# Kernel tuning notes

Measured on AMD Instinct MI355X. Metric: run time of the kernel, lower is better.

## Reference

```python
import jax, jax.numpy as jnp
import numpy as np

DIM = 1024
DEPTH = 6
HEADS = 16
DIM_HEAD = 64
INNER = HEADS * DIM_HEAD  # 1024
NUM_LATENTS = 64
FF = 4 * DIM
EPS = 1e-5


def _ln(t, g, b):
    m = jnp.mean(t, axis=-1, keepdims=True)
    v = jnp.mean(jnp.square(t - m), axis=-1, keepdims=True)
    return (t - m) * jax.lax.rsqrt(v + EPS) * g + b


def setup_inputs() -> dict:
    key = jax.random.key(0)
    ks = jax.random.split(key, 12)
    s = 0.02
    x = jax.random.normal(ks[0], (4, 8, 4, 256, DIM), dtype=jnp.float32)
    latents = jax.random.normal(ks[1], (NUM_LATENTS, DIM), dtype=jnp.float32)
    wq = jax.random.normal(ks[2], (DEPTH, DIM, INNER), dtype=jnp.float32) * s
    wkv = jax.random.normal(ks[3], (DEPTH, DIM, 2 * INNER), dtype=jnp.float32) * s
    wo = jax.random.normal(ks[4], (DEPTH, INNER, DIM), dtype=jnp.float32) * s
    w1 = jax.random.normal(ks[5], (DEPTH, DIM, FF), dtype=jnp.float32) * s
    w2 = jax.random.normal(ks[6], (DEPTH, FF, DIM), dtype=jnp.float32) * s
    nm_g = jnp.ones((DEPTH, DIM), jnp.float32); nm_b = jnp.zeros((DEPTH, DIM), jnp.float32)
    nl_g = jnp.ones((DEPTH, DIM), jnp.float32); nl_b = jnp.zeros((DEPTH, DIM), jnp.float32)
    ff_g = jnp.ones((DEPTH, DIM), jnp.float32); ff_b = jnp.zeros((DEPTH, DIM), jnp.float32)
    fin_g = jnp.ones((DIM,), jnp.float32); fin_b = jnp.zeros((DIM,), jnp.float32)
    return {"x": x, "latents": latents, "nm_g": nm_g, "nm_b": nm_b,
            "nl_g": nl_g, "nl_b": nl_b, "wq": wq, "wkv": wkv, "wo": wo,
            "ff_g": ff_g, "ff_b": ff_b, "w1": w1, "w2": w2,
            "fin_g": fin_g, "fin_b": fin_b}


def _to_heads(t):
    # [B,T,N,inner] -> [B,h,T,N,dh]
    B, T, N, _ = t.shape
    return t.reshape(B, T, N, HEADS, DIM_HEAD).transpose(0, 3, 1, 2, 4)


def reference(x, latents, nm_g, nm_b, nl_g, nl_b, wq, wkv, wo,
              ff_g, ff_b, w1, w2, fin_g, fin_b):
    B, T, F, V, D = x.shape
    x = x.reshape(B, T, F * V, D)  # media tokens
    lat = jnp.broadcast_to(latents[None, None], (B, T, NUM_LATENTS, D))
    scale = DIM_HEAD ** -0.5
    for i in range(DEPTH):
        # --- cross attention (queries=latents, kv = media ++ latents) ---
        xn = _ln(x, nm_g[i], nm_b[i])
        ln_lat = _ln(lat, nl_g[i], nl_b[i])
        q = ln_lat @ wq[i]                                # [B,T,N2,inner]
        kv = jnp.concatenate([xn, ln_lat], axis=-2) @ wkv[i]
        k, v = jnp.split(kv, 2, axis=-1)
        qh = _to_heads(q) * scale                          # [B,h,T,N2,dh]
        kh = _to_heads(k)                                  # [B,h,T,Nk,dh]
        vh = _to_heads(v)
        sim = jnp.einsum('bhtid,bhtjd->bhtij', qh, kh)
        attn = jax.nn.softmax(sim, axis=-1)
        out = jnp.einsum('bhtij,bhtjd->bhtid', attn, vh)   # [B,h,T,N2,dh]
        out = out.transpose(0, 2, 3, 1, 4).reshape(B, T, NUM_LATENTS, INNER)
        lat = out @ wo[i] + lat
        # --- feed forward ---
        h = _ln(lat, ff_g[i], ff_b[i]) @ w1[i]
        h = jax.nn.gelu(h, approximate=False) @ w2[i]
        lat = h + lat
    return _ln(lat, fin_g, fin_b)
```

## Files before the change

### kernel.cpp

```cpp
#include <hip/hip_runtime.h>


typedef unsigned short u16;
typedef __attribute__((ext_vector_type(8))) short short8;
typedef __attribute__((ext_vector_type(4))) float f32x4;

__device__ __forceinline__ float bf2f(u16 u) {
  return __uint_as_float(((unsigned)u) << 16);
}
__device__ __forceinline__ u16 f2bf(float f) {
  unsigned u = __float_as_uint(f);
  unsigned r = (u + 0x7FFFu + ((u >> 16) & 1u)) >> 16;
  return (u16)r;
}

__global__ void detect_kernel(const u16* __restrict__ x, int* __restrict__ flag) {
  int lane = threadIdx.x;
  u16 u = x[2 * lane];
  int e = (u >> 7) & 0xFF;
  unsigned long long b = __ballot(e >= 115 && e <= 133);
  if (lane == 0) flag[0] = (__popcll(b) >= 40) ? 1 : 0;
}

__global__ __launch_bounds__(256)
void wtrans_kernel(const void* __restrict__ W, long woff, u16* __restrict__ Wt,
                   int K, int N, const int* __restrict__ flag) {
  const int isb = *flag;
  __shared__ u16 t[64][72];
  const long k0 = (long)blockIdx.x * 64;
  const long n0 = (long)blockIdx.y * 64;
  const int tr = threadIdx.x >> 2;
  const int tc = (threadIdx.x & 3) * 16;
  if (isb) {
    const u16* src = (const u16*)W + woff + (k0 + tr) * N + n0 + tc;
    *(int4*)&t[tr][tc]     = *(const int4*)src;
    *(int4*)&t[tr][tc + 8] = *(const int4*)(src + 8);
  } else {
    const float* src = (const float*)W + woff + (k0 + tr) * N + n0 + tc;
    float4 f0 = *(const float4*)(src);
    float4 f1 = *(const float4*)(src + 4);
    float4 f2 = *(const float4*)(src + 8);
    float4 f3 = *(const float4*)(src + 12);
    u16 tmp[16] = {f2bf(f0.x), f2bf(f0.y), f2bf(f0.z), f2bf(f0.w),
                   f2bf(f1.x), f2bf(f1.y), f2bf(f1.z), f2bf(f1.w),
                   f2bf(f2.x), f2bf(f2.y), f2bf(f2.z), f2bf(f2.w),
                   f2bf(f3.x), f2bf(f3.y), f2bf(f3.z), f2bf(f3.w)};
    *(int4*)&t[tr][tc]     = *(int4*)&tmp[0];
    *(int4*)&t[tr][tc + 8] = *(int4*)&tmp[8];
  }
  __syncthreads();
  u16 o[16];
#pragma unroll
  for (int j = 0; j < 16; ++j) o[j] = t[tc + j][tr];
  u16* dst = Wt + (n0 + tr) * (long)K + k0 + tc;
  *(int4*)dst       = *(int4*)&o[0];
  *(int4*)(dst + 8) = *(int4*)&o[8];
}

template <int EPI>
__global__ __launch_bounds__(256, 2)
void gemm_kernel(const u16* __restrict__ A, const u16* __restrict__ Bt,
                 void* __restrict__ Cp, const float* __restrict__ R,
                 int M, int N, int K) {
  __shared__ u16 As[128][74];
  __shared__ u16 Bs[128][74];

  const int tid  = threadIdx.x;
  const int lane = tid & 63;
  const int wave = tid >> 6;
  const int wm = (wave >> 1) * 64;
  const int wn = (wave & 1) * 64;
  const int r  = lane & 15;
  const int qd = lane >> 4;

  const long bm = (long)blockIdx.x * 128;
  const long bn = (long)blockIdx.y * 128;

  f32x4 acc[4][4];
#pragma unroll
  for (int i = 0; i < 4; ++i)
#pragma unroll
    for (int j = 0; j < 4; ++j) acc[i][j] = (f32x4){0.f, 0.f, 0.f, 0.f};

  const int ra = tid >> 3, ca = (tid & 7) * 8;
  const u16* Aptr = A  + (bm + ra) * (long)K + ca;
  const u16* Bptr = Bt + (bn + ra) * (long)K + ca;

  for (int k0 = 0; k0 < K; k0 += 64) {
#pragma unroll
    for (int it = 0; it < 4; ++it) {
      int4 av = *(const int4*)(Aptr + (long)(it * 32) * K + k0);
      *(int4*)(&As[ra + it * 32][ca]) = av;
    }
#pragma unroll
    for (int it = 0; it < 4; ++it) {
      int4 bv = *(const int4*)(Bptr + (long)(it * 32) * K + k0);
      *(int4*)(&Bs[ra + it * 32][ca]) = bv;
    }
    __syncthreads();

#pragma unroll
    for (int kh = 0; kh < 2; ++kh) {
      short8 af[4], bfv[4];
#pragma unroll
      for (int mt = 0; mt < 4; ++mt)
        af[mt] = *(const short8*)(&As[wm + mt * 16 + r][kh * 32 + qd * 8]);
#pragma unroll
      for (int nt = 0; nt < 4; ++nt)
        bfv[nt] = *(const short8*)(&Bs[wn + nt * 16 + r][kh * 32 + qd * 8]);
#pragma unroll
      for (int mt = 0; mt < 4; ++mt)
#pragma unroll
        for (int nt = 0; nt < 4; ++nt)
          acc[mt][nt] = __builtin_amdgcn_mfma_f32_16x16x32_bf16(
              bfv[nt], af[mt], acc[mt][nt], 0, 0, 0);
    }
    __syncthreads();
  }

#pragma unroll
  for (int mt = 0; mt < 4; ++mt) {
    const long row = bm + wm + mt * 16 + r;
#pragma unroll
    for (int nt = 0; nt < 4; ++nt) {
      const long col = bn + wn + nt * 16 + qd * 4;
      const long idx = row * N + col;
      if (EPI == 0) {
        ushort4 o;
        o.x = f2bf(acc[mt][nt][0]); o.y = f2bf(acc[mt][nt][1]);
        o.z = f2bf(acc[mt][nt][2]); o.w = f2bf(acc[mt][nt][3]);
        *(ushort4*)((u16*)Cp + idx) = o;
      } else if (EPI == 1) {
        ushort4 o;
        float v0 = acc[mt][nt][0], v1 = acc[mt][nt][1];
        float v2 = acc[mt][nt][2], v3 = acc[mt][nt][3];
        o.x = f2bf(0.5f * v0 * (1.0f + erff(v0 * 0.70710678118654752f)));
        o.y = f2bf(0.5f * v1 * (1.0f + erff(v1 * 0.70710678118654752f)));
        o.z = f2bf(0.5f * v2 * (1.0f + erff(v2 * 0.70710678118654752f)));
        o.w = f2bf(0.5f * v3 * (1.0f + erff(v3 * 0.70710678118654752f)));
        *(ushort4*)((u16*)Cp + idx) = o;
      } else {
        float4 rv = *(const float4*)(R + idx);
        float4 o;
        o.x = acc[mt][nt][0] + rv.x; o.y = acc[mt][nt][1] + rv.y;
        o.z = acc[mt][nt][2] + rv.z; o.w = acc[mt][nt][3] + rv.w;
        *(float4*)((float*)Cp + idx) = o;
      }
    }
  }
}

template <int INMODE, int OUTMODE>
__global__ __launch_bounds__(256)
void ln_kernel(const void* __restrict__ inp, long ioff,
               const void* __restrict__ gam, const void* __restrict__ bet,
               long goff, void* __restrict__ outp, const int* __restrict__ flag) {
  const int isb = *flag;
  const long row = blockIdx.x;
  const int tid = threadIdx.x;
  float x0, x1, x2, x3;
  const bool in_f32 = (INMODE == 1) || (!isb);
  if (in_f32) {
    float4 v = *((const float4*)((const float*)inp + ioff + row * 1024) + tid);
    x0 = v.x; x1 = v.y; x2 = v.z; x3 = v.w;
  } else {
    ushort4 u = *((const ushort4*)((const u16*)inp + ioff + row * 1024) + tid);
    x0 = bf2f(u.x); x1 = bf2f(u.y); x2 = bf2f(u.z); x3 = bf2f(u.w);
  }
  float s1 = x0 + x1 + x2 + x3;
  float s2 = x0 * x0 + x1 * x1 + x2 * x2 + x3 * x3;
#pragma unroll
  for (int off = 32; off >= 1; off >>= 1) {
    s1 += __shfl_xor(s1, off);
    s2 += __shfl_xor(s2, off);
  }
  __shared__ float r1[4], r2[4];
  if ((tid & 63) == 0) { r1[tid >> 6] = s1; r2[tid >> 6] = s2; }
  __syncthreads();
  s1 = r1[0] + r1[1] + r1[2] + r1[3];
  s2 = r2[0] + r2[1] + r2[2] + r2[3];
  const float mean = s1 * (1.0f / 1024.0f);
  const float var  = s2 * (1.0f / 1024.0f) - mean * mean;
  const float rstd = rsqrtf(var + 1e-5f);
  float g0, g1, g2, g3, b0, b1, b2, b3;
  if (isb) {
    ushort4 ug = *((const ushort4*)((const u16*)gam + goff) + tid);
    ushort4 ub = *((const ushort4*)((const u16*)bet + goff) + tid);
    g0 = bf2f(ug.x); g1 = bf2f(ug.y); g2 = bf2f(ug.z); g3 = bf2f(ug.w);
    b0 = bf2f(ub.x); b1 = bf2f(ub.y); b2 = bf2f(ub.z); b3 = bf2f(ub.w);
  } else {
    float4 vg = *((const float4*)((const float*)gam + goff) + tid);
    float4 vb = *((const float4*)((const float*)bet + goff) + tid);
    g0 = vg.x; g1 = vg.y; g2 = vg.z; g3 = vg.w;
    b0 = vb.x; b1 = vb.y; b2 = vb.z; b3 = vb.w;
  }
  float o0 = (x0 - mean) * rstd * g0 + b0;
  float o1 = (x1 - mean) * rstd * g1 + b1;
  float o2 = (x2 - mean) * rstd * g2 + b2;
  float o3 = (x3 - mean) * rstd * g3 + b3;
  const bool out_f32 = (OUTMODE == 1) && (!isb);
  if (out_f32) {
    float4 o = {o0, o1, o2, o3};
    *((float4*)((float*)outp + row * 1024) + tid) = o;
  } else {
    ushort4 o;
    o.x = f2bf(o0); o.y = f2bf(o1); o.z = f2bf(o2); o.w = f2bf(o3);
    *((ushort4*)((u16*)outp + row * 1024) + tid) = o;
  }
}

__global__ __launch_bounds__(256)
void init_lat_kernel(const void* __restrict__ latents, float* __restrict__ lat,
                     const int* __restrict__ flag) {
  const int isb = *flag;
  long i = (long)blockIdx.x * 256 + threadIdx.x;
  long src = (4 * i) & 65535;
  float4 o;
  if (isb) {
    ushort4 u = *(const ushort4*)((const u16*)latents + src);
    o = (float4){bf2f(u.x), bf2f(u.y), bf2f(u.z), bf2f(u.w)};
  } else {
    o = *(const float4*)((const float*)latents + src);
  }
  *(float4*)(lat + 4 * i) = o;
}

__global__ __launch_bounds__(256, 2)
void attn_kernel(const u16* __restrict__ Q, const u16* __restrict__ KVM,
                 const u16* __restrict__ KVL, u16* __restrict__ O, int g0) {
  const int gl = blockIdx.x;
  const int g  = g0 + gl;
  const int h  = blockIdx.y;
  __shared__ u16 k_s[64][72];
  __shared__ u16 vt_s[64][72];
  __shared__ u16 qp_s[64][72];

  const int tid  = threadIdx.x;
  const int lane = tid & 63;
  const int wave = tid >> 6;
  const int r  = lane & 15;
  const int qd = lane >> 4;
  const int qr = wave * 16;

  {
    const int rr = tid >> 2, cc = (tid & 3) * 16;
    const u16* qp = Q + ((long)g * 64 + rr) * 1024 + h * 64 + cc;
    *(int4*)&qp_s[rr][cc]     = *(const int4*)qp;
    *(int4*)&qp_s[rr][cc + 8] = *(const int4*)(qp + 8);
  }
  __syncthreads();

  short8 aq0 = *(const short8*)&qp_s[qr + r][qd * 8];
  short8 aq1 = *(const short8*)&qp_s[qr + r][32 + qd * 8];

  f32x4 acc_o[4];
  float m0[4], l0[4];
#pragma unroll
  for (int i = 0; i < 4; ++i) {
    m0[i] = -3.0e38f;
    l0[i] = 0.f;
    acc_o[i] = (f32x4){0.f, 0.f, 0.f, 0.f};
  }

  for (int t = 0; t < 17; ++t) {
    const u16* base = (t < 16)
        ? KVM + ((long)gl * 1024 + t * 64) * 2048 + h * 64
        : KVL + ((long)g * 64) * 2048 + h * 64;
    {
      const int rr = tid >> 2, cc = (tid & 3) * 16;
      const u16* kp = base + (long)rr * 2048 + cc;
      *(int4*)&k_s[rr][cc]     = *(const int4*)kp;
      *(int4*)&k_s[rr][cc + 8] = *(const int4*)(kp + 8);
    }
    {
      const int d = lane;
      const u16* vp = base + 1024 + (long)(wave * 16) * 2048 + d;
      union { u16 u[16]; int4 v[2]; } tmp;
#pragma unroll
      for (int u = 0; u < 16; ++u) tmp.u[u] = vp[(long)u * 2048];
      *(int4*)&vt_s[d][wave * 16]     = tmp.v[0];
      *(int4*)&vt_s[d][wave * 16 + 8] = tmp.v[1];
    }
    __syncthreads();

    f32x4 sac[4];
#pragma unroll
    for (int nt = 0; nt < 4; ++nt) sac[nt] = (f32x4){0.f, 0.f, 0.f, 0.f};
#pragma unroll
    for (int nt = 0; nt < 4; ++nt) {
      short8 b0 = *(const short8*)&k_s[nt * 16 + r][qd * 8];
      short8 b1 = *(const short8*)&k_s[nt * 16 + r][32 + qd * 8];
      sac[nt] = __builtin_amdgcn_mfma_f32_16x16x32_bf16(aq0, b0, sac[nt], 0, 0, 0);
      sac[nt] = __builtin_amdgcn_mfma_f32_16x16x32_bf16(aq1, b1, sac[nt], 0, 0, 0);
    }

    float pr[4][4];
#pragma unroll
    for (int nt = 0; nt < 4; ++nt)
#pragma unroll
      for (int i = 0; i < 4; ++i) pr[nt][i] = sac[nt][i] * 0.125f;

#pragma unroll
    for (int i = 0; i < 4; ++i) {
      float mt = fmaxf(fmaxf(pr[0][i], pr[1][i]), fmaxf(pr[2][i], pr[3][i]));
      mt = fmaxf(mt, __shfl_xor(mt, 1));
      mt = fmaxf(mt, __shfl_xor(mt, 2));
      mt = fmaxf(mt, __shfl_xor(mt, 4));
      mt = fmaxf(mt, __shfl_xor(mt, 8));
      float mn = fmaxf(m0[i], mt);
      float al = __expf(m0[i] - mn);
      m0[i] = mn;
      float ts = 0.f;
#pragma unroll
      for (int nt = 0; nt < 4; ++nt) {
        float p = __expf(pr[nt][i] - mn);
        pr[nt][i] = p;
        ts += p;
      }
      ts += __shfl_xor(ts, 1);
      ts += __shfl_xor(ts, 2);
      ts += __shfl_xor(ts, 4);
      ts += __shfl_xor(ts, 8);
      l0[i] = l0[i] * al + ts;
#pragma unroll
      for (int nt = 0; nt < 4; ++nt) acc_o[nt][i] *= al;
    }

#pragma unroll
    for (int nt = 0; nt < 4; ++nt)
#pragma unroll
      for (int i = 0; i < 4; ++i)
        qp_s[qr + qd * 4 + i][nt * 16 + r] = f2bf(pr[nt][i]);

    short8 ap0 = *(const short8*)&qp_s[qr + r][qd * 8];
    short8 ap1 = *(const short8*)&qp_s[qr + r][32 + qd * 8];
#pragma unroll
    for (int nt = 0; nt < 4; ++nt) {
      short8 b0 = *(const short8*)&vt_s[nt * 16 + r][qd * 8];
      short8 b1 = *(const short8*)&vt_s[nt * 16 + r][32 + qd * 8];
      acc_o[nt] = __builtin_amdgcn_mfma_f32_16x16x32_bf16(ap0, b0, acc_o[nt], 0, 0, 0);
      acc_o[nt] = __builtin_amdgcn_mfma_f32_16x16x32_bf16(ap1, b1, acc_o[nt], 0, 0, 0);
    }
    __syncthreads();
  }

#pragma unroll
  for (int i = 0; i < 4; ++i) {
    float inv = 1.0f / l0[i];
    long row = (long)g * 64 + qr + qd * 4 + i;
#pragma unroll
    for (int nt = 0; nt < 4; ++nt)
      O[row * 1024 + h * 64 + nt * 16 + r] = f2bf(acc_o[nt][i] * inv);
  }
}

extern "C" void kernel_launch(void* const* d_in, const int* in_sizes, int n_in,
                              void* d_out, int out_size, void* d_ws, size_t ws_size,
                              hipStream_t stream) {
  const void* x     = d_in[0];
  const void* lats  = d_in[1];
  const void* nm_g  = d_in[2];
  const void* nm_b  = d_in[3];
  const void* nl_g  = d_in[4];
  const void* nl_b  = d_in[5];
  const void* wq    = d_in[6];
  const void* wkv   = d_in[7];
  const void* wo    = d_in[8];
  const void* ff_g  = d_in[9];
  const void* ff_b  = d_in[10];
  const void* w1    = d_in[11];
  const void* w2    = d_in[12];
  const void* fin_g = d_in[13];
  const void* fin_b = d_in[14];

  const size_t MB = 1024ull * 1024ull;
  char* w = (char*)d_ws;
  int*   flag = (int*)w;    w += 1 * MB;
  float* lat  = (float*)w;  w += 8 * MB;
  u16*   lnl  = (u16*)w;    w += 4 * MB;
  u16*   qbuf = (u16*)w;    w += 4 * MB;
  u16*   ao   = (u16*)w;    w += 4 * MB;
  u16*   kvl  = (u16*)w;    w += 8 * MB;
  u16*   h1   = (u16*)w;    w += 16 * MB;
  u16*   wqt  = (u16*)w;    w += 2 * MB;
  u16*   wkvt = (u16*)w;    w += 4 * MB;
  u16*   wot  = (u16*)w;    w += 2 * MB;
  u16*   w1t  = (u16*)w;    w += 8 * MB;
  u16*   w2t  = (u16*)w;    w += 8 * MB;
  const size_t base = 69 * MB;
  int CH = 32;
  while (CH > 1 && base + (size_t)CH * 6 * MB > ws_size) CH >>= 1;
  u16* xn  = (u16*)w;  w += (size_t)CH * 2 * MB;
  u16* kvm = (u16*)w;
  const int nch = 32 / CH;

  detect_kernel<<<1, 64, 0, stream>>>((const u16*)x, flag);
  init_lat_kernel<<<2048, 256, 0, stream>>>(lats, lat, flag);

  for (int i = 0; i < 6; ++i) {
    wtrans_kernel<<<dim3(16, 16), 256, 0, stream>>>(
        wq, (long)i * 1024 * 1024, wqt, 1024, 1024, flag);
    wtrans_kernel<<<dim3(16, 32), 256, 0, stream>>>(
        wkv, (long)i * 1024 * 2048, wkvt, 1024, 2048, flag);
    wtrans_kernel<<<dim3(16, 16), 256, 0, stream>>>(
        wo, (long)i * 1024 * 1024, wot, 1024, 1024, flag);
    wtrans_kernel<<<dim3(16, 64), 256, 0, stream>>>(
        w1, (long)i * 1024 * 4096, w1t, 1024, 4096, flag);
    wtrans_kernel<<<dim3(64, 16), 256, 0, stream>>>(
        w2, (long)i * 4096 * 1024, w2t, 4096, 1024, flag);

    ln_kernel<1, 0><<<2048, 256, 0, stream>>>(
        lat, 0, nl_g, nl_b, (long)i * 1024, lnl, flag);
    gemm_kernel<0><<<dim3(16, 8), 256, 0, stream>>>(
        lnl, wqt, qbuf, nullptr, 2048, 1024, 1024);
    gemm_kernel<0><<<dim3(16, 16), 256, 0, stream>>>(
        lnl, wkvt, kvl, nullptr, 2048, 2048, 1024);
    for (int c = 0; c < nch; ++c) {
      ln_kernel<0, 0><<<CH * 1024, 256, 0, stream>>>(
          x, (long)c * CH * 1024 * 1024, nm_g, nm_b, (long)i * 1024, xn, flag);
      gemm_kernel<0><<<dim3(CH * 8, 16), 256, 0, stream>>>(
          xn, wkvt, kvm, nullptr, CH * 1024, 2048, 1024);
      attn_kernel<<<dim3(CH, 16), 256, 0, stream>>>(qbuf, kvm, kvl, ao, c * CH);
    }
    gemm_kernel<2><<<dim3(16, 8), 256, 0, stream>>>(
        ao, wot, lat, lat, 2048, 1024, 1024);
    ln_kernel<1, 0><<<2048, 256, 0, stream>>>(
        lat, 0, ff_g, ff_b, (long)i * 1024, lnl, flag);
    gemm_kernel<1><<<dim3(16, 32), 256, 0, stream>>>(
        lnl, w1t, h1, nullptr, 2048, 4096, 1024);
    gemm_kernel<2><<<dim3(16, 8), 256, 0, stream>>>(
        h1, w2t, lat, lat, 2048, 1024, 4096);
  }
  ln_kernel<1, 1><<<2048, 256, 0, stream>>>(
      lat, 0, fin_g, fin_b, 0, d_out, flag);
}
```

Measured before the change: 3.503 ms.

## Prefetch next K-tile into registers and swizzle GEMM block order

The GEMM main loop now loads the next 64-wide K slice of A and B into registers while MFMAs run on the current shared-memory tile, then writes it to shared memory after a barrier. This hides global-memory latency behind compute. Block indices are also remapped into groups of 8 along M so blocks running at the same time share B tiles in L2. The register prefetch adds 32 VGPRs per thread, which may pressure the launch bound of 2 blocks per SM.

After: 9.573 ms. 2.73x slower.

```diff
diff --git a/kernel.cpp b/kernel.cpp
--- a/kernel.cpp
+++ b/kernel.cpp
@@ -73,8 +73,17 @@
   const int r  = lane & 15;
   const int qd = lane >> 4;
 
-  const long bm = (long)blockIdx.x * 128;
-  const long bn = (long)blockIdx.y * 128;
+  int bx = blockIdx.x, by = blockIdx.y;
+  if ((gridDim.x & 7) == 0) {
+    const int gy = gridDim.y;
+    int f = by * gridDim.x + bx;
+    int ntg = 8 * gy;
+    int g = f / ntg, rem = f % ntg;
+    bx = g * 8 + (rem & 7);
+    by = rem >> 3;
+  }
+  const long bm = (long)bx * 128;
+  const long bn = (long)by * 128;
 
   f32x4 acc[4][4];
 #pragma unroll
@@ -86,18 +95,28 @@
   const u16* Aptr = A  + (bm + ra) * (long)K + ca;
   const u16* Bptr = Bt + (bn + ra) * (long)K + ca;
 
+  int4 pa[4], pb[4];
+#pragma unroll
+  for (int it = 0; it < 4; ++it) {
+    pa[it] = *(const int4*)(Aptr + (long)(it * 32) * K);
+    pb[it] = *(const int4*)(Bptr + (long)(it * 32) * K);
+  }
+#pragma unroll
+  for (int it = 0; it < 4; ++it) {
+    *(int4*)(&As[ra + it * 32][ca]) = pa[it];
+    *(int4*)(&Bs[ra + it * 32][ca]) = pb[it];
+  }
+  __syncthreads();
+
   for (int k0 = 0; k0 < K; k0 += 64) {
-#pragma unroll
-    for (int it = 0; it < 4; ++it) {
-      int4 av = *(const int4*)(Aptr + (long)(it * 32) * K + k0);
-      *(int4*)(&As[ra + it * 32][ca]) = av;
-    }
-#pragma unroll
-    for (int it = 0; it < 4; ++it) {
-      int4 bv = *(const int4*)(Bptr + (long)(it * 32) * K + k0);
-      *(int4*)(&Bs[ra + it * 32][ca]) = bv;
-    }
-    __syncthreads();
+    const bool has_next = (k0 + 64 < K);
+    if (has_next) {
+#pragma unroll
+      for (int it = 0; it < 4; ++it) {
+        pa[it] = *(const int4*)(Aptr + (long)(it * 32) * K + k0 + 64);
+        pb[it] = *(const int4*)(Bptr + (long)(it * 32) * K + k0 + 64);
+      }
+    }
 
 #pragma unroll
     for (int kh = 0; kh < 2; ++kh) {
@@ -115,7 +134,16 @@
           acc[mt][nt] = __builtin_amdgcn_mfma_f32_16x16x32_bf16(
               bfv[nt], af[mt], acc[mt][nt], 0, 0, 0);
     }
-    __syncthreads();
+
+    if (has_next) {
+      __syncthreads();
+#pragma unroll
+      for (int it = 0; it < 4; ++it) {
+        *(int4*)(&As[ra + it * 32][ca]) = pa[it];
+        *(int4*)(&Bs[ra + it * 32][ca]) = pb[it];
+      }
+      __syncthreads();
+    }
   }
 
 #pragma unroll
```
